# Kernel tuning notes

Hardware: AMD Instinct MI355X
Metric: run time of the kernel (lower is better)

Reference implementation:

```python
import jax, jax.numpy as jnp
import numpy as np

S = 4096      # total packed tokens
B = 8         # number of variable-length segments
E = 1152      # embed_dim (SigLIP2 so400m)
H = 16        # num_heads
D = E // H    # head_dim = 72


def setup_inputs() -> dict:
    key = jax.random.key(0)
    ks = jax.random.split(key, 8)
    w_std = 0.02
    theta = jax.random.uniform(ks[1], (S, D), jnp.float32, 0.0, 2.0 * np.pi)
    return {
        "hidden_states": jax.random.normal(ks[0], (S, E), jnp.float32),
        "cu_seqlens": jnp.arange(B + 1, dtype=jnp.int32) * (S // B),
        "cos": jnp.cos(theta),
        "sin": jnp.sin(theta),
        "Wq": jax.random.normal(ks[2], (E, E), jnp.float32) * w_std,
        "bq": jnp.zeros((E,), jnp.float32),
        "Wk": jax.random.normal(ks[3], (E, E), jnp.float32) * w_std,
        "bk": jnp.zeros((E,), jnp.float32),
        "Wv": jax.random.normal(ks[4], (E, E), jnp.float32) * w_std,
        "bv": jnp.zeros((E,), jnp.float32),
        "Wo": jax.random.normal(ks[5], (E, E), jnp.float32) * w_std,
        "bo": jnp.zeros((E,), jnp.float32),
    }


def _rotate_half(x):
    x1, x2 = jnp.split(x, 2, axis=-1)
    return jnp.concatenate((-x2, x1), axis=-1)


def reference(hidden_states, cu_seqlens, cos, sin, Wq, bq, Wk, bk, Wv, bv, Wo, bo):
    seq_len = hidden_states.shape[0]
    scale = np.float32(D) ** -0.5
    # projections -> [S, H, D]
    q = (hidden_states @ Wq.T + bq).reshape(seq_len, H, D)
    k = (hidden_states @ Wk.T + bk).reshape(seq_len, H, D)
    v = (hidden_states @ Wv.T + bv).reshape(seq_len, H, D)
    # inline RoPE (apply_rotary_pos_emb_vision): cos/sin broadcast over heads
    c = cos[:, None, :]
    s = sin[:, None, :]
    q = q * c + _rotate_half(q) * s
    k = k * c + _rotate_half(k) * s
    # segment id per token from cu_seqlens; block-diagonal attention mask
    seg = jnp.searchsorted(cu_seqlens[1:], jnp.arange(seq_len, dtype=cu_seqlens.dtype), side="right")
    mask = seg[:, None] == seg[None, :]                     # [S, S]
    scores = jnp.einsum("shd,thd->hst", q, k) * scale       # [H, S, S]
    neg = jnp.finfo(scores.dtype).min
    scores = jnp.where(mask[None, :, :], scores, neg)
    probs = jax.nn.softmax(scores, axis=-1)
    attn = jnp.einsum("hst,thd->shd", probs, v).reshape(seq_len, E)
    return attn @ Wo.T + bo
```

## Files before the change

kernel.cpp:

```cpp
#include <hip/hip_runtime.h>
#include <float.h>

#define S_LEN 4096
#define E_DIM 1152
#define NH    16
#define HD    72
#define HD2   36
#define NQKV  3456

typedef __attribute__((ext_vector_type(4))) float f32x4;
typedef __attribute__((ext_vector_type(8))) _Float16 f16x8;

__device__ __forceinline__ unsigned short f2h(float f) {
    union { _Float16 h; unsigned short u; } c;
    c.h = (_Float16)f;
    return c.u;
}

__device__ __forceinline__ void gload_lds16(const unsigned short* g, unsigned short* l) {
    __builtin_amdgcn_global_load_lds(
        (const __attribute__((address_space(1))) unsigned int*)g,
        (__attribute__((address_space(3))) unsigned int*)l, 16, 0, 0);
}

__global__ __launch_bounds__(256)
void pack_f16(const float* __restrict__ hs, const float* __restrict__ wq,
              const float* __restrict__ wk, const float* __restrict__ wv,
              const float* __restrict__ wo,
              unsigned short* __restrict__ hs_h, unsigned short* __restrict__ wqkv_h,
              unsigned short* __restrict__ wo_h)
{
    const float* src; unsigned short* dst; int n4;
    const int WSZ = E_DIM * E_DIM;
    switch (blockIdx.z) {
        case 0: src = hs; dst = hs_h;             n4 = S_LEN * E_DIM / 4; break;
        case 1: src = wq; dst = wqkv_h;           n4 = WSZ / 4; break;
        case 2: src = wk; dst = wqkv_h + WSZ;     n4 = WSZ / 4; break;
        case 3: src = wv; dst = wqkv_h + 2 * WSZ; n4 = WSZ / 4; break;
        default: src = wo; dst = wo_h;            n4 = WSZ / 4; break;
    }
    for (int i = blockIdx.x * 256 + threadIdx.x; i < n4; i += gridDim.x * 256) {
        f32x4 x = ((const f32x4*)src)[i];
        ushort4 hv;
        hv.x = f2h(x[0]); hv.y = f2h(x[1]); hv.z = f2h(x[2]); hv.w = f2h(x[3]);
        ((ushort4*)dst)[i] = hv;
    }
}

__global__ __launch_bounds__(256, 4)
void gemm_qkv_f16(const unsigned short* __restrict__ Ah, const unsigned short* __restrict__ Wh,
                  const float* __restrict__ bq, const float* __restrict__ bk,
                  const float* __restrict__ bv,
                  float* __restrict__ oq, float* __restrict__ ok,
                  unsigned short* __restrict__ vt)
{
    __shared__ unsigned short sA[128 * 64];
    __shared__ unsigned short sB[128 * 64];
    const int tid  = threadIdx.x;
    const int w    = tid >> 6, lane = tid & 63;
    const int quad = lane >> 4, m = lane & 15;
    const int wr   = w & 1,  wc = w >> 1;

    const int bid = blockIdx.x;
    const int lin = (bid & 7) * 108 + (bid >> 3);
    const int n_t = lin >> 5;
    const int m_t = lin & 31;
    const int m0  = m_t * 128;
    const int n0  = n_t * 128;

    const int srow = lane >> 3;
    const int skc  = (lane & 7) ^ srow;

    f32x4 acc[4][4];
    #pragma unroll
    for (int i = 0; i < 4; ++i)
        #pragma unroll
        for (int j = 0; j < 4; ++j) acc[i][j] = (f32x4){0.f, 0.f, 0.f, 0.f};

    const int rm7 = m & 7;

    for (int k0 = 0; k0 < E_DIM; k0 += 64) {
        #pragma unroll
        for (int c = 0; c < 4; ++c) {
            int r = 32 * w + 8 * c + srow;
            gload_lds16(Ah + (size_t)(m0 + r) * E_DIM + k0 + skc * 8, &sA[(32 * w + 8 * c) * 64]);
            gload_lds16(Wh + (size_t)(n0 + r) * E_DIM + k0 + skc * 8, &sB[(32 * w + 8 * c) * 64]);
        }
        __syncthreads();

        #pragma unroll
        for (int k3 = 0; k3 < 2; ++k3) {
            f16x8 ah[4], bh[4];
            #pragma unroll
            for (int t = 0; t < 4; ++t) {
                int pc = ((k3 << 2) + quad) ^ rm7;
                ah[t] = *(const f16x8*)&sA[(64 * wr + 16 * t + m) * 64 + pc * 8];
                bh[t] = *(const f16x8*)&sB[(64 * wc + 16 * t + m) * 64 + pc * 8];
            }
            #pragma unroll
            for (int rt = 0; rt < 4; ++rt)
                #pragma unroll
                for (int ct = 0; ct < 4; ++ct)
                    acc[rt][ct] = __builtin_amdgcn_mfma_f32_16x16x32_f16(ah[rt], bh[ct], acc[rt][ct], 0, 0, 0);
        }
        __syncthreads();
    }

    const int which = n0 / E_DIM;
    const int n0l = n0 - which * E_DIM;
    if (which < 2) {
        const float* bp = (which == 0) ? bq : bk;
        float* Cp       = (which == 0) ? oq : ok;
        #pragma unroll
        for (int ct = 0; ct < 4; ++ct) {
            int col = n0l + 64 * wc + 16 * ct + m;
            float bias = bp[col];
            #pragma unroll
            for (int rt = 0; rt < 4; ++rt)
                #pragma unroll
                for (int reg = 0; reg < 4; ++reg) {
                    int row = m0 + 64 * wr + 16 * rt + 4 * quad + reg;
                    Cp[(size_t)row * E_DIM + col] = acc[rt][ct][reg] + bias;
                }
        }
    } else {
        #pragma unroll
        for (int ct = 0; ct < 4; ++ct) {
            int vcol = n0l + 64 * wc + 16 * ct + m;
            int hh = vcol / HD, dd = vcol - hh * HD;
            float bias = bv[vcol];
            unsigned short* vrow = vt + ((size_t)hh * HD + dd) * S_LEN;
            #pragma unroll
            for (int rt = 0; rt < 4; ++rt) {
                int s0r = m0 + 64 * wr + 16 * rt + 4 * quad;
                ushort4 o;
                o.x = f2h(acc[rt][ct][0] + bias);
                o.y = f2h(acc[rt][ct][1] + bias);
                o.z = f2h(acc[rt][ct][2] + bias);
                o.w = f2h(acc[rt][ct][3] + bias);
                *(ushort4*)&vrow[s0r] = o;
            }
        }
    }
}

__global__ __launch_bounds__(256, 4)
void gemm_out_f16(const unsigned short* __restrict__ Ah, const unsigned short* __restrict__ Wh,
                  const float* __restrict__ bo, float* __restrict__ Cp)
{
    __shared__ unsigned short sA[64 * 64];
    __shared__ unsigned short sB[128 * 64];
    const int tid  = threadIdx.x;
    const int w    = tid >> 6, lane = tid & 63;
    const int quad = lane >> 4, m = lane & 15;
    const int m0   = blockIdx.y * 64;
    const int n0   = blockIdx.x * 128;

    const int srow = lane >> 3;
    const int skc  = (lane & 7) ^ srow;

    f32x4 acc[4][2];
    #pragma unroll
    for (int i = 0; i < 4; ++i)
        #pragma unroll
        for (int j = 0; j < 2; ++j) acc[i][j] = (f32x4){0.f, 0.f, 0.f, 0.f};

    const int rm7 = m & 7;

    for (int k0 = 0; k0 < E_DIM; k0 += 64) {
        #pragma unroll
        for (int c = 0; c < 2; ++c) {
            int r = 16 * w + 8 * c + srow;
            gload_lds16(Ah + (size_t)(m0 + r) * E_DIM + k0 + skc * 8, &sA[(16 * w + 8 * c) * 64]);
        }
        #pragma unroll
        for (int c = 0; c < 4; ++c) {
            int r = 32 * w + 8 * c + srow;
            gload_lds16(Wh + (size_t)(n0 + r) * E_DIM + k0 + skc * 8, &sB[(32 * w + 8 * c) * 64]);
        }
        __syncthreads();
        #pragma unroll
        for (int k3 = 0; k3 < 2; ++k3) {
            f16x8 ah[4], bh[2];
            int pc = ((k3 << 2) + quad) ^ rm7;
            #pragma unroll
            for (int t = 0; t < 4; ++t)
                ah[t] = *(const f16x8*)&sA[(16 * t + m) * 64 + pc * 8];
            #pragma unroll
            for (int ct = 0; ct < 2; ++ct)
                bh[ct] = *(const f16x8*)&sB[(32 * w + 16 * ct + m) * 64 + pc * 8];
            #pragma unroll
            for (int rt = 0; rt < 4; ++rt)
                #pragma unroll
                for (int ct = 0; ct < 2; ++ct)
                    acc[rt][ct] = __builtin_amdgcn_mfma_f32_16x16x32_f16(ah[rt], bh[ct], acc[rt][ct], 0, 0, 0);
        }
        __syncthreads();
    }

    #pragma unroll
    for (int ct = 0; ct < 2; ++ct) {
        int col = n0 + 32 * w + 16 * ct + m;
        float bias = bo[col];
        #pragma unroll
        for (int rt = 0; rt < 4; ++rt)
            #pragma unroll
            for (int reg = 0; reg < 4; ++reg) {
                int row = m0 + 16 * rt + 4 * quad + reg;
                Cp[(size_t)row * E_DIM + col] = acc[rt][ct][reg] + bias;
            }
    }
}

__global__ __launch_bounds__(256)
void prep_k(const float* __restrict__ kf, const float* __restrict__ cosb,
            const float* __restrict__ sinb, unsigned short* __restrict__ kh)
{
    const int h  = blockIdx.y;
    const int s0 = blockIdx.x * 64;
    for (int task = threadIdx.x; task < 64 * 9; task += 256) {
        int row = task / 9, d0 = (task % 9) << 2;
        int s = s0 + row;
        const float* xr = kf + (size_t)s * E_DIM + h * HD;
        f32x4 a  = *(const f32x4*)(xr + d0);
        f32x4 b  = *(const f32x4*)(xr + d0 + HD2);
        f32x4 c1 = *(const f32x4*)(cosb + (size_t)s * HD + d0);
        f32x4 s1 = *(const f32x4*)(sinb + (size_t)s * HD + d0);
        f32x4 c2 = *(const f32x4*)(cosb + (size_t)s * HD + d0 + HD2);
        f32x4 s2 = *(const f32x4*)(sinb + (size_t)s * HD + d0 + HD2);
        f32x4 r1 = a * c1 - b * s1;
        f32x4 r2 = b * c2 + a * s2;
        uint2 u1, u2;
        u1.x = (unsigned)f2h(r1[0]) | ((unsigned)f2h(r1[1]) << 16);
        u1.y = (unsigned)f2h(r1[2]) | ((unsigned)f2h(r1[3]) << 16);
        u2.x = (unsigned)f2h(r2[0]) | ((unsigned)f2h(r2[1]) << 16);
        u2.y = (unsigned)f2h(r2[2]) | ((unsigned)f2h(r2[3]) << 16);
        unsigned short* orow = kh + ((size_t)h * S_LEN + s) * HD;
        *(uint2*)&orow[d0]       = u1;
        *(uint2*)&orow[d0 + HD2] = u2;
    }
}

__global__ __launch_bounds__(256, 4)
void attn_f16(const float* __restrict__ qf, const float* __restrict__ cosb,
              const float* __restrict__ sinb, const unsigned short* __restrict__ kh,
              const unsigned short* __restrict__ vt, const int* __restrict__ cu,
              int nseg, unsigned short* __restrict__ out)
{
    __shared__ unsigned short ks_s[64][72];
    __shared__ unsigned short vs_s[80][72];
    __shared__ unsigned short ss_s[64][72];

    const int tid  = threadIdx.x;
    const int w    = tid >> 6;
    const int lane = tid & 63;
    const int quad = lane >> 4;
    const int m    = lane & 15;
    const int h    = blockIdx.y;
    const int qb0  = blockIdx.x * 64;
    const float cexp = 0.17002324f;

    {
        uint4 zz = make_uint4(0u, 0u, 0u, 0u);
        if (tid < 72) {
            int r = 72 + tid / 9, c = tid % 9;
            *(uint4*)&vs_s[r][c << 3] = zz;
        }
    }

    int rs_r[4], re_r[4];
    #pragma unroll
    for (int reg = 0; reg < 4; ++reg) {
        int row = qb0 + 16 * w + 4 * quad + reg;
        int st = 0;
        for (int i = 1; i < nseg; ++i) if (cu[i] <= row) st = i;
        rs_r[reg] = cu[st];
        re_r[reg] = cu[st + 1];
    }
    int st0 = 0, st1 = 0;
    for (int i = 1; i < nseg; ++i) {
        if (cu[i] <= qb0) st0 = i;
        if (cu[i] <= qb0 + 63) st1 = i;
    }
    const int kstart = cu[st0];
    const int kend   = cu[st1 + 1];
    const bool aligned = (st0 == st1);

    const unsigned short* ktbase = kh + (size_t)h * S_LEN * HD;
    const unsigned short* vtbase = vt + (size_t)h * HD * S_LEN;
    unsigned short* ksf = &ks_s[0][0];

    const int sl0 = tid, sl1 = tid + 256;
    const int sl2 = (tid < 64) ? tid + 512 : tid + 256;
    const int vd0 = sl0 >> 3, vc0 = (sl0 & 7) << 3;
    const int vd1 = sl1 >> 3, vc1 = (sl1 & 7) << 3;
    const int vd2 = sl2 >> 3, vc2 = (sl2 & 7) << 3;

    uint4 kp0, kp1, kp2, vp0, vp1, vp2;
    {
        const unsigned short* kt = ktbase + (size_t)kstart * HD;
        kp0 = *(const uint4*)(kt + sl0 * 8);
        kp1 = *(const uint4*)(kt + sl1 * 8);
        kp2 = *(const uint4*)(kt + sl2 * 8);
        vp0 = *(const uint4*)(vtbase + (size_t)vd0 * S_LEN + kstart + vc0);
        vp1 = *(const uint4*)(vtbase + (size_t)vd1 * S_LEN + kstart + vc1);
        vp2 = *(const uint4*)(vtbase + (size_t)vd2 * S_LEN + kstart + vc2);
    }

    for (int task = tid; task < 64 * 9; task += 256) {
        int row = task / 9, d0 = (task % 9) << 2;
        int s = qb0 + row;
        const float* xr = qf + (size_t)s * E_DIM + h * HD;
        f32x4 a  = *(const f32x4*)(xr + d0);
        f32x4 b  = *(const f32x4*)(xr + d0 + HD2);
        f32x4 c1 = *(const f32x4*)(cosb + (size_t)s * HD + d0);
        f32x4 s1 = *(const f32x4*)(sinb + (size_t)s * HD + d0);
        f32x4 c2 = *(const f32x4*)(cosb + (size_t)s * HD + d0 + HD2);
        f32x4 s2 = *(const f32x4*)(sinb + (size_t)s * HD + d0 + HD2);
        f32x4 r1 = a * c1 - b * s1;
        f32x4 r2 = b * c2 + a * s2;
        uint2 u1, u2;
        u1.x = (unsigned)f2h(r1[0]) | ((unsigned)f2h(r1[1]) << 16);
        u1.y = (unsigned)f2h(r1[2]) | ((unsigned)f2h(r1[3]) << 16);
        u2.x = (unsigned)f2h(r2[0]) | ((unsigned)f2h(r2[1]) << 16);
        u2.y = (unsigned)f2h(r2[2]) | ((unsigned)f2h(r2[3]) << 16);
        *(uint2*)&ks_s[row][d0]       = u1;
        *(uint2*)&ks_s[row][d0 + HD2] = u2;
    }
    __syncthreads();

    f16x8 qfr[3];
    {
        const unsigned short* qrow = &ks_s[16 * w + m][0];
        #pragma unroll
        for (int k3 = 0; k3 < 3; ++k3) {
            bool pad = (k3 == 2) && (quad != 0);
            int off = pad ? 0 : (k3 * 32 + quad * 8);
            f16x8 val = *(const f16x8*)(qrow + off);
            f16x8 z = {0, 0, 0, 0, 0, 0, 0, 0};
            qfr[k3] = pad ? z : val;
        }
    }

    f32x4 acc_o[5];
    #pragma unroll
    for (int i = 0; i < 5; ++i) acc_o[i] = (f32x4){0.f, 0.f, 0.f, 0.f};
    float l_r[4] = {0.f, 0.f, 0.f, 0.f};

    for (int kb = kstart; kb < kend; kb += 64) {
        __syncthreads();
        *(uint4*)(ksf + sl0 * 8) = kp0;
        *(uint4*)(ksf + sl1 * 8) = kp1;
        if (tid < 64) *(uint4*)(ksf + sl2 * 8) = kp2;
        *(uint4*)&vs_s[vd0][vc0] = vp0;
        *(uint4*)&vs_s[vd1][vc1] = vp1;
        if (tid < 64) *(uint4*)&vs_s[vd2][vc2] = vp2;
        __syncthreads();

        int kn = kb + 64;
        if (kn < kend) {
            const unsigned short* kt = ktbase + (size_t)kn * HD;
            kp0 = *(const uint4*)(kt + sl0 * 8);
            kp1 = *(const uint4*)(kt + sl1 * 8);
            kp2 = *(const uint4*)(kt + sl2 * 8);
            vp0 = *(const uint4*)(vtbase + (size_t)vd0 * S_LEN + kn + vc0);
            vp1 = *(const uint4*)(vtbase + (size_t)vd1 * S_LEN + kn + vc1);
            vp2 = *(const uint4*)(vtbase + (size_t)vd2 * S_LEN + kn + vc2);
        }

        f32x4 sacc[4];
        #pragma unroll
        for (int ct = 0; ct < 4; ++ct) sacc[ct] = (f32x4){0.f, 0.f, 0.f, 0.f};
        #pragma unroll
        for (int ct = 0; ct < 4; ++ct) {
            const unsigned short* krow = &ks_s[16 * ct + m][0];
            #pragma unroll
            for (int k3 = 0; k3 < 3; ++k3) {
                bool pad = (k3 == 2) && (quad != 0);
                int off = pad ? 0 : (k3 * 32 + quad * 8);
                f16x8 bfr = *(const f16x8*)(krow + off);
                f16x8 z = {0, 0, 0, 0, 0, 0, 0, 0};
                bfr = pad ? z : bfr;
                sacc[ct] = __builtin_amdgcn_mfma_f32_16x16x32_f16(qfr[k3], bfr, sacc[ct], 0, 0, 0);
            }
        }

        if (aligned) {
            #pragma unroll
            for (int ct = 0; ct < 4; ++ct)
                #pragma unroll
                for (int reg = 0; reg < 4; ++reg) {
                    float p = __builtin_amdgcn_exp2f(sacc[ct][reg] * cexp);
                    l_r[reg] += p;
                    ss_s[16 * w + 4 * quad + reg][16 * ct + m] = f2h(p);
                }
        } else {
            #pragma unroll
            for (int ct = 0; ct < 4; ++ct) {
                int key = kb + 16 * ct + m;
                #pragma unroll
                for (int reg = 0; reg < 4; ++reg) {
                    bool valid = (key >= rs_r[reg]) && (key < re_r[reg]);
                    float p = valid ? __builtin_amdgcn_exp2f(sacc[ct][reg] * cexp) : 0.f;
                    l_r[reg] += p;
                    ss_s[16 * w + 4 * quad + reg][16 * ct + m] = f2h(p);
                }
            }
        }

        {
            const unsigned short* prow = &ss_s[16 * w + m][0];
            f16x8 pf0 = *(const f16x8*)(prow + quad * 8);
            f16x8 pf1 = *(const f16x8*)(prow + 32 + quad * 8);
            #pragma unroll
            for (int ct2 = 0; ct2 < 5; ++ct2) {
                const unsigned short* vrow = &vs_s[16 * ct2 + m][0];
                f16x8 vf0 = *(const f16x8*)(vrow + quad * 8);
                f16x8 vf1 = *(const f16x8*)(vrow + 32 + quad * 8);
                acc_o[ct2] = __builtin_amdgcn_mfma_f32_16x16x32_f16(pf0, vf0, acc_o[ct2], 0, 0, 0);
                acc_o[ct2] = __builtin_amdgcn_mfma_f32_16x16x32_f16(pf1, vf1, acc_o[ct2], 0, 0, 0);
            }
        }
    }

    #pragma unroll
    for (int reg = 0; reg < 4; ++reg) {
        float l = l_r[reg];
        l += __shfl_xor(l, 1);
        l += __shfl_xor(l, 2);
        l += __shfl_xor(l, 4);
        l += __shfl_xor(l, 8);
        l_r[reg] = l;
    }

    #pragma unroll
    for (int reg = 0; reg < 4; ++reg) {
        float linv = (l_r[reg] > 0.f) ? 1.f / l_r[reg] : 0.f;
        int row = qb0 + 16 * w + 4 * quad + reg;
        unsigned short* orow = out + (size_t)row * E_DIM + h * HD;
        #pragma unroll
        for (int ct2 = 0; ct2 < 5; ++ct2) {
            int col = 16 * ct2 + m;
            if (col < HD) orow[col] = f2h(acc_o[ct2][reg] * linv);
        }
    }
}

extern "C" void kernel_launch(void* const* d_in, const int* in_sizes, int n_in,
                              void* d_out, int out_size, void* d_ws, size_t ws_size,
                              hipStream_t stream)
{
    const float* hs   = (const float*)d_in[0];
    const int*   cu   = (const int*)d_in[1];
    const float* cosb = (const float*)d_in[2];
    const float* sinb = (const float*)d_in[3];
    const float* Wq   = (const float*)d_in[4];
    const float* bq   = (const float*)d_in[5];
    const float* Wk   = (const float*)d_in[6];
    const float* bk   = (const float*)d_in[7];
    const float* Wv   = (const float*)d_in[8];
    const float* bv   = (const float*)d_in[9];
    const float* Wo   = (const float*)d_in[10];
    const float* bo   = (const float*)d_in[11];
    float* outp = (float*)d_out;

    const size_t mat = (size_t)S_LEN * E_DIM;
    float* qf = (float*)d_ws;
    float* kf = qf + mat;
    unsigned short* hs_h   = (unsigned short*)(kf + mat);
    unsigned short* wqkv_h = hs_h + mat;
    unsigned short* wo_h   = wqkv_h + (size_t)NQKV * E_DIM;
    unsigned short* vtb    = wo_h + (size_t)E_DIM * E_DIM;
    unsigned short* kh     = hs_h;
    unsigned short* attn_h = (unsigned short*)kf;

    const int nseg = in_sizes[1] - 1;

    dim3 gpack(512, 1, 5);
    pack_f16<<<gpack, 256, 0, stream>>>(hs, Wq, Wk, Wv, Wo, hs_h, wqkv_h, wo_h);

    gemm_qkv_f16<<<dim3(864), 256, 0, stream>>>(hs_h, wqkv_h, bq, bk, bv, qf, kf, vtb);

    dim3 gprep(S_LEN / 64, NH, 1);
    prep_k<<<gprep, 256, 0, stream>>>(kf, cosb, sinb, kh);

    dim3 gattn(S_LEN / 64, NH, 1);
    attn_f16<<<gattn, 256, 0, stream>>>(qf, cosb, sinb, kh, vtb, cu, nseg, attn_h);

    dim3 gout(E_DIM / 128, S_LEN / 64, 1);
    gemm_out_f16<<<gout, 256, 0, stream>>>(attn_h, wo_h, bo, outp);
}
```

Measured before the change: 207.3 us.

## Fuse RoPE and f16 conversion of Q/K into QKV GEMM epilogue

Permutes the Wq/Wk rows during packing so each rotate-half pair lands in adjacent output columns. The QKV GEMM epilogue can then apply RoPE with a lane shuffle and write head-major f16 Q and K directly. This removes the fp32 Q/K round trip, the separate prep_k kernel and the in-attention Q RoPE pass. The cost is scattered 2-byte stores, per-element cos/sin loads in the epilogue, and index arithmetic in the packing loop.

```diff
diff --git a/kernel.cpp b/kernel.cpp
--- a/kernel.cpp
+++ b/kernel.cpp
@@ -32,18 +32,27 @@
 {
     const float* src; unsigned short* dst; int n4;
     const int WSZ = E_DIM * E_DIM;
-    switch (blockIdx.z) {
+    const int z = blockIdx.z;
+    switch (z) {
         case 0: src = hs; dst = hs_h;             n4 = S_LEN * E_DIM / 4; break;
         case 1: src = wq; dst = wqkv_h;           n4 = WSZ / 4; break;
         case 2: src = wk; dst = wqkv_h + WSZ;     n4 = WSZ / 4; break;
         case 3: src = wv; dst = wqkv_h + 2 * WSZ; n4 = WSZ / 4; break;
         default: src = wo; dst = wo_h;            n4 = WSZ / 4; break;
     }
+    const bool perm = (z == 1) || (z == 2);
     for (int i = blockIdx.x * 256 + threadIdx.x; i < n4; i += gridDim.x * 256) {
         f32x4 x = ((const f32x4*)src)[i];
         ushort4 hv;
         hv.x = f2h(x[0]); hv.y = f2h(x[1]); hv.z = f2h(x[2]); hv.w = f2h(x[3]);
-        ((ushort4*)dst)[i] = hv;
+        int o = i;
+        if (perm) {
+            int r = i / 288, cc = i - r * 288;
+            int hh = r / HD, p0 = r - hh * HD;
+            int pr = hh * HD + ((p0 < HD2) ? (p0 << 1) : (((p0 - HD2) << 1) | 1));
+            o = pr * 288 + cc;
+        }
+        ((ushort4*)dst)[o] = hv;
     }
 }
 
@@ -51,7 +60,8 @@
 void gemm_qkv_f16(const unsigned short* __restrict__ Ah, const unsigned short* __restrict__ Wh,
                   const float* __restrict__ bq, const float* __restrict__ bk,
                   const float* __restrict__ bv,
-                  float* __restrict__ oq, float* __restrict__ ok,
+                  const float* __restrict__ cosb, const float* __restrict__ sinb,
+                  unsigned short* __restrict__ qh, unsigned short* __restrict__ khp,
                   unsigned short* __restrict__ vt)
 {
     __shared__ unsigned short sA[128 * 64];
@@ -109,18 +119,26 @@
     const int which = n0 / E_DIM;
     const int n0l = n0 - which * E_DIM;
     if (which < 2) {
-        const float* bp = (which == 0) ? bq : bk;
-        float* Cp       = (which == 0) ? oq : ok;
+        unsigned short* dst = (which == 0) ? qh : khp;
+        const float* bp     = (which == 0) ? bq : bk;
         #pragma unroll
         for (int ct = 0; ct < 4; ++ct) {
-            int col = n0l + 64 * wc + 16 * ct + m;
-            float bias = bp[col];
+            int c = n0l + 64 * wc + 16 * ct + m;
+            int hh = c / HD, p = c - hh * HD;
+            int cidx = (p >> 1) + ((p & 1) ? HD2 : 0);
+            float bias = bp[hh * HD + cidx];
+            float sgn  = (p & 1) ? 1.f : -1.f;
+            unsigned short* hcol = dst + (size_t)hh * S_LEN * HD + p;
             #pragma unroll
             for (int rt = 0; rt < 4; ++rt)
                 #pragma unroll
                 for (int reg = 0; reg < 4; ++reg) {
-                    int row = m0 + 64 * wr + 16 * rt + 4 * quad + reg;
-                    Cp[(size_t)row * E_DIM + col] = acc[rt][ct][reg] + bias;
+                    int s = m0 + 64 * wr + 16 * rt + 4 * quad + reg;
+                    float v  = acc[rt][ct][reg] + bias;
+                    float pv = __shfl_xor(v, 1);
+                    float cs = cosb[(size_t)s * HD + cidx];
+                    float sn = sinb[(size_t)s * HD + cidx];
+                    hcol[(size_t)s * HD] = f2h(v * cs + sgn * pv * sn);
                 }
         }
     } else {
@@ -212,38 +230,8 @@
     }
 }
 
-__global__ __launch_bounds__(256)
-void prep_k(const float* __restrict__ kf, const float* __restrict__ cosb,
-            const float* __restrict__ sinb, unsigned short* __restrict__ kh)
-{
-    const int h  = blockIdx.y;
-    const int s0 = blockIdx.x * 64;
-    for (int task = threadIdx.x; task < 64 * 9; task += 256) {
-        int row = task / 9, d0 = (task % 9) << 2;
-        int s = s0 + row;
-        const float* xr = kf + (size_t)s * E_DIM + h * HD;
-        f32x4 a  = *(const f32x4*)(xr + d0);
-        f32x4 b  = *(const f32x4*)(xr + d0 + HD2);
-        f32x4 c1 = *(const f32x4*)(cosb + (size_t)s * HD + d0);
-        f32x4 s1 = *(const f32x4*)(sinb + (size_t)s * HD + d0);
-        f32x4 c2 = *(const f32x4*)(cosb + (size_t)s * HD + d0 + HD2);
-        f32x4 s2 = *(const f32x4*)(sinb + (size_t)s * HD + d0 + HD2);
-        f32x4 r1 = a * c1 - b * s1;
-        f32x4 r2 = b * c2 + a * s2;
-        uint2 u1, u2;
-        u1.x = (unsigned)f2h(r1[0]) | ((unsigned)f2h(r1[1]) << 16);
-        u1.y = (unsigned)f2h(r1[2]) | ((unsigned)f2h(r1[3]) << 16);
-        u2.x = (unsigned)f2h(r2[0]) | ((unsigned)f2h(r2[1]) << 16);
-        u2.y = (unsigned)f2h(r2[2]) | ((unsigned)f2h(r2[3]) << 16);
-        unsigned short* orow = kh + ((size_t)h * S_LEN + s) * HD;
-        *(uint2*)&orow[d0]       = u1;
-        *(uint2*)&orow[d0 + HD2] = u2;
-    }
-}
-
 __global__ __launch_bounds__(256, 4)
-void attn_f16(const float* __restrict__ qf, const float* __restrict__ cosb,
-              const float* __restrict__ sinb, const unsigned short* __restrict__ kh,
+void attn_f16(const unsigned short* __restrict__ qh, const unsigned short* __restrict__ kh,
               const unsigned short* __restrict__ vt, const int* __restrict__ cu,
               int nseg, unsigned short* __restrict__ out)
 {
@@ -307,31 +295,9 @@
         vp2 = *(const uint4*)(vtbase + (size_t)vd2 * S_LEN + kstart + vc2);
     }
 
-    for (int task = tid; task < 64 * 9; task += 256) {
-        int row = task / 9, d0 = (task % 9) << 2;
-        int s = qb0 + row;
-        const float* xr = qf + (size_t)s * E_DIM + h * HD;
-        f32x4 a  = *(const f32x4*)(xr + d0);
-        f32x4 b  = *(const f32x4*)(xr + d0 + HD2);
-        f32x4 c1 = *(const f32x4*)(cosb + (size_t)s * HD + d0);
-        f32x4 s1 = *(const f32x4*)(sinb + (size_t)s * HD + d0);
-        f32x4 c2 = *(const f32x4*)(cosb + (size_t)s * HD + d0 + HD2);
-        f32x4 s2 = *(const f32x4*)(sinb + (size_t)s * HD + d0 + HD2);
-        f32x4 r1 = a * c1 - b * s1;
-        f32x4 r2 = b * c2 + a * s2;
-        uint2 u1, u2;
-        u1.x = (unsigned)f2h(r1[0]) | ((unsigned)f2h(r1[1]) << 16);
-        u1.y = (unsigned)f2h(r1[2]) | ((unsigned)f2h(r1[3]) << 16);
-        u2.x = (unsigned)f2h(r2[0]) | ((unsigned)f2h(r2[1]) << 16);
-        u2.y = (unsigned)f2h(r2[2]) | ((unsigned)f2h(r2[3]) << 16);
-        *(uint2*)&ks_s[row][d0]       = u1;
-        *(uint2*)&ks_s[row][d0 + HD2] = u2;
-    }
-    __syncthreads();
-
     f16x8 qfr[3];
     {
-        const unsigned short* qrow = &ks_s[16 * w + m][0];
+        const unsigned short* qrow = qh + ((size_t)h * S_LEN + qb0 + 16 * w + m) * HD;
         #pragma unroll
         for (int k3 = 0; k3 < 3; ++k3) {
             bool pad = (k3 == 2) && (quad != 0);
@@ -465,27 +431,24 @@
     float* outp = (float*)d_out;
 
     const size_t mat = (size_t)S_LEN * E_DIM;
-    float* qf = (float*)d_ws;
-    float* kf = qf + mat;
-    unsigned short* hs_h   = (unsigned short*)(kf + mat);
+    unsigned short* hs_h   = (unsigned short*)d_ws;
     unsigned short* wqkv_h = hs_h + mat;
     unsigned short* wo_h   = wqkv_h + (size_t)NQKV * E_DIM;
     unsigned short* vtb    = wo_h + (size_t)E_DIM * E_DIM;
-    unsigned short* kh     = hs_h;
-    unsigned short* attn_h = (unsigned short*)kf;
+    unsigned short* qh     = vtb + mat;
+    unsigned short* kh     = qh + mat;
+    unsigned short* attn_h = kh + mat;
 
     const int nseg = in_sizes[1] - 1;
 
     dim3 gpack(512, 1, 5);
     pack_f16<<<gpack, 256, 0, stream>>>(hs, Wq, Wk, Wv, Wo, hs_h, wqkv_h, wo_h);
 
-    gemm_qkv_f16<<<dim3(864), 256, 0, stream>>>(hs_h, wqkv_h, bq, bk, bv, qf, kf, vtb);
-
-    dim3 gprep(S_LEN / 64, NH, 1);
-    prep_k<<<gprep, 256, 0, stream>>>(kf, cosb, sinb, kh);
+    gemm_qkv_f16<<<dim3(864), 256, 0, stream>>>(hs_h, wqkv_h, bq, bk, bv,
+                                                cosb, sinb, qh, kh, vtb);
 
     dim3 gattn(S_LEN / 64, NH, 1);
-    attn_f16<<<gattn, 256, 0, stream>>>(qf, cosb, sinb, kh, vtb, cu, nseg, attn_h);
+    attn_f16<<<gattn, 256, 0, stream>>>(qh, kh, vtb, cu, nseg, attn_h);
 
     dim3 gout(E_DIM / 128, S_LEN / 64, 1);
     gemm_out_f16<<<gout, 256, 0, stream>>>(attn_h, wo_h, bo, outp);
```

Result: slower. 212.0 us (+2.3%).

## Process two 64-row query tiles per attention block to reuse K/V tiles

Applied to the files above, without the earlier changes.

Each attention workgroup now handles 128 query rows as two 64-row sub-tiles that share every K/V tile staged in LDS. This halves the global-to-LDS K/V traffic and barrier count per query row. In exchange it doubles the accumulator and Q-fragment registers, relaxes the launch bound from 4 to 3 blocks per CU, and halves the grid to 512 blocks, which may lower occupancy and latency hiding.

```diff
diff --git a/kernel.cpp b/kernel.cpp
--- a/kernel.cpp
+++ b/kernel.cpp
@@ -241,7 +241,7 @@
     }
 }
 
-__global__ __launch_bounds__(256, 4)
+__global__ __launch_bounds__(256, 3)
 void attn_f16(const float* __restrict__ qf, const float* __restrict__ cosb,
               const float* __restrict__ sinb, const unsigned short* __restrict__ kh,
               const unsigned short* __restrict__ vt, const int* __restrict__ cu,
@@ -257,7 +257,7 @@
     const int quad = lane >> 4;
     const int m    = lane & 15;
     const int h    = blockIdx.y;
-    const int qb0  = blockIdx.x * 64;
+    const int qb0  = blockIdx.x * 128;
     const float cexp = 0.17002324f;
 
     {
@@ -268,19 +268,21 @@
         }
     }
 
-    int rs_r[4], re_r[4];
-    #pragma unroll
-    for (int reg = 0; reg < 4; ++reg) {
-        int row = qb0 + 16 * w + 4 * quad + reg;
-        int st = 0;
-        for (int i = 1; i < nseg; ++i) if (cu[i] <= row) st = i;
-        rs_r[reg] = cu[st];
-        re_r[reg] = cu[st + 1];
-    }
+    int rs_r[2][4], re_r[2][4];
+    #pragma unroll
+    for (int t = 0; t < 2; ++t)
+        #pragma unroll
+        for (int reg = 0; reg < 4; ++reg) {
+            int row = qb0 + 64 * t + 16 * w + 4 * quad + reg;
+            int st = 0;
+            for (int i = 1; i < nseg; ++i) if (cu[i] <= row) st = i;
+            rs_r[t][reg] = cu[st];
+            re_r[t][reg] = cu[st + 1];
+        }
     int st0 = 0, st1 = 0;
     for (int i = 1; i < nseg; ++i) {
         if (cu[i] <= qb0) st0 = i;
-        if (cu[i] <= qb0 + 63) st1 = i;
+        if (cu[i] <= qb0 + 127) st1 = i;
     }
     const int kstart = cu[st0];
     const int kend   = cu[st1 + 1];
@@ -307,30 +309,31 @@
         vp2 = *(const uint4*)(vtbase + (size_t)vd2 * S_LEN + kstart + vc2);
     }
 
-    for (int task = tid; task < 64 * 9; task += 256) {
-        int row = task / 9, d0 = (task % 9) << 2;
-        int s = qb0 + row;
-        const float* xr = qf + (size_t)s * E_DIM + h * HD;
-        f32x4 a  = *(const f32x4*)(xr + d0);
-        f32x4 b  = *(const f32x4*)(xr + d0 + HD2);
-        f32x4 c1 = *(const f32x4*)(cosb + (size_t)s * HD + d0);
-        f32x4 s1 = *(const f32x4*)(sinb + (size_t)s * HD + d0);
-        f32x4 c2 = *(const f32x4*)(cosb + (size_t)s * HD + d0 + HD2);
-        f32x4 s2 = *(const f32x4*)(sinb + (size_t)s * HD + d0 + HD2);
-        f32x4 r1 = a * c1 - b * s1;
-        f32x4 r2 = b * c2 + a * s2;
-        uint2 u1, u2;
-        u1.x = (unsigned)f2h(r1[0]) | ((unsigned)f2h(r1[1]) << 16);
-        u1.y = (unsigned)f2h(r1[2]) | ((unsigned)f2h(r1[3]) << 16);
-        u2.x = (unsigned)f2h(r2[0]) | ((unsigned)f2h(r2[1]) << 16);
-        u2.y = (unsigned)f2h(r2[2]) | ((unsigned)f2h(r2[3]) << 16);
-        *(uint2*)&ks_s[row][d0]       = u1;
-        *(uint2*)&ks_s[row][d0 + HD2] = u2;
-    }
-    __syncthreads();
-
-    f16x8 qfr[3];
-    {
+    f16x8 qfr[2][3];
+    #pragma unroll
+    for (int t = 0; t < 2; ++t) {
+        if (t) __syncthreads();
+        for (int task = tid; task < 64 * 9; task += 256) {
+            int row = task / 9, d0 = (task % 9) << 2;
+            int s = qb0 + 64 * t + row;
+            const float* xr = qf + (size_t)s * E_DIM + h * HD;
+            f32x4 a  = *(const f32x4*)(xr + d0);
+            f32x4 b  = *(const f32x4*)(xr + d0 + HD2);
+            f32x4 c1 = *(const f32x4*)(cosb + (size_t)s * HD + d0);
+            f32x4 s1 = *(const f32x4*)(sinb + (size_t)s * HD + d0);
+            f32x4 c2 = *(const f32x4*)(cosb + (size_t)s * HD + d0 + HD2);
+            f32x4 s2 = *(const f32x4*)(sinb + (size_t)s * HD + d0 + HD2);
+            f32x4 r1 = a * c1 - b * s1;
+            f32x4 r2 = b * c2 + a * s2;
+            uint2 u1, u2;
+            u1.x = (unsigned)f2h(r1[0]) | ((unsigned)f2h(r1[1]) << 16);
+            u1.y = (unsigned)f2h(r1[2]) | ((unsigned)f2h(r1[3]) << 16);
+            u2.x = (unsigned)f2h(r2[0]) | ((unsigned)f2h(r2[1]) << 16);
+            u2.y = (unsigned)f2h(r2[2]) | ((unsigned)f2h(r2[3]) << 16);
+            *(uint2*)&ks_s[row][d0]       = u1;
+            *(uint2*)&ks_s[row][d0 + HD2] = u2;
+        }
+        __syncthreads();
         const unsigned short* qrow = &ks_s[16 * w + m][0];
         #pragma unroll
         for (int k3 = 0; k3 < 3; ++k3) {
@@ -338,14 +341,16 @@
             int off = pad ? 0 : (k3 * 32 + quad * 8);
             f16x8 val = *(const f16x8*)(qrow + off);
             f16x8 z = {0, 0, 0, 0, 0, 0, 0, 0};
-            qfr[k3] = pad ? z : val;
-        }
-    }
-
-    f32x4 acc_o[5];
-    #pragma unroll
-    for (int i = 0; i < 5; ++i) acc_o[i] = (f32x4){0.f, 0.f, 0.f, 0.f};
-    float l_r[4] = {0.f, 0.f, 0.f, 0.f};
+            qfr[t][k3] = pad ? z : val;
+        }
+    }
+
+    f32x4 acc_o[2][5];
+    #pragma unroll
+    for (int t = 0; t < 2; ++t)
+        #pragma unroll
+        for (int i = 0; i < 5; ++i) acc_o[t][i] = (f32x4){0.f, 0.f, 0.f, 0.f};
+    float l_r[2][4] = {{0.f, 0.f, 0.f, 0.f}, {0.f, 0.f, 0.f, 0.f}};
 
     for (int kb = kstart; kb < kend; kb += 64) {
         __syncthreads();
@@ -368,82 +373,89 @@
             vp2 = *(const uint4*)(vtbase + (size_t)vd2 * S_LEN + kn + vc2);
         }
 
-        f32x4 sacc[4];
-        #pragma unroll
-        for (int ct = 0; ct < 4; ++ct) sacc[ct] = (f32x4){0.f, 0.f, 0.f, 0.f};
-        #pragma unroll
-        for (int ct = 0; ct < 4; ++ct) {
-            const unsigned short* krow = &ks_s[16 * ct + m][0];
-            #pragma unroll
-            for (int k3 = 0; k3 < 3; ++k3) {
-                bool pad = (k3 == 2) && (quad != 0);
-                int off = pad ? 0 : (k3 * 32 + quad * 8);
-                f16x8 bfr = *(const f16x8*)(krow + off);
-                f16x8 z = {0, 0, 0, 0, 0, 0, 0, 0};
-                bfr = pad ? z : bfr;
-                sacc[ct] = __builtin_amdgcn_mfma_f32_16x16x32_f16(qfr[k3], bfr, sacc[ct], 0, 0, 0);
-            }
-        }
-
-        if (aligned) {
-            #pragma unroll
-            for (int ct = 0; ct < 4; ++ct)
-                #pragma unroll
-                for (int reg = 0; reg < 4; ++reg) {
-                    float p = __builtin_amdgcn_exp2f(sacc[ct][reg] * cexp);
-                    l_r[reg] += p;
-                    ss_s[16 * w + 4 * quad + reg][16 * ct + m] = f2h(p);
+        #pragma unroll
+        for (int t = 0; t < 2; ++t) {
+            f32x4 sacc[4];
+            #pragma unroll
+            for (int ct = 0; ct < 4; ++ct) sacc[ct] = (f32x4){0.f, 0.f, 0.f, 0.f};
+            #pragma unroll
+            for (int ct = 0; ct < 4; ++ct) {
+                const unsigned short* krow = &ks_s[16 * ct + m][0];
+                #pragma unroll
+                for (int k3 = 0; k3 < 3; ++k3) {
+                    bool pad = (k3 == 2) && (quad != 0);
+                    int off = pad ? 0 : (k3 * 32 + quad * 8);
+                    f16x8 bfr = *(const f16x8*)(krow + off);
+                    f16x8 z = {0, 0, 0, 0, 0, 0, 0, 0};
+                    bfr = pad ? z : bfr;
+                    sacc[ct] = __builtin_amdgcn_mfma_f32_16x16x32_f16(qfr[t][k3], bfr, sacc[ct], 0, 0, 0);
                 }
-        } else {
-            #pragma unroll
-            for (int ct = 0; ct < 4; ++ct) {
-                int key = kb + 16 * ct + m;
-                #pragma unroll
-                for (int reg = 0; reg < 4; ++reg) {
-                    bool valid = (key >= rs_r[reg]) && (key < re_r[reg]);
-                    float p = valid ? __builtin_amdgcn_exp2f(sacc[ct][reg] * cexp) : 0.f;
-                    l_r[reg] += p;
-                    ss_s[16 * w + 4 * quad + reg][16 * ct + m] = f2h(p);
+            }
+
+            if (aligned) {
+                #pragma unroll
+                for (int ct = 0; ct < 4; ++ct)
+                    #pragma unroll
+                    for (int reg = 0; reg < 4; ++reg) {
+                        float p = __builtin_amdgcn_exp2f(sacc[ct][reg] * cexp);
+                        l_r[t][reg] += p;
+                        ss_s[16 * w + 4 * quad + reg][16 * ct + m] = f2h(p);
+                    }
+            } else {
+                #pragma unroll
+                for (int ct = 0; ct < 4; ++ct) {
+                    int key = kb + 16 * ct + m;
+                    #pragma unroll
+                    for (int reg = 0; reg < 4; ++reg) {
+                        bool valid = (key >= rs_r[t][reg]) && (key < re_r[t][reg]);
+                        float p = valid ? __builtin_amdgcn_exp2f(sacc[ct][reg] * cexp) : 0.f;
+                        l_r[t][reg] += p;
+                        ss_s[16 * w + 4 * quad + reg][16 * ct + m] = f2h(p);
+                    }
                 }
             }
-        }
-
-        {
-            const unsigned short* prow = &ss_s[16 * w + m][0];
-            f16x8 pf0 = *(const f16x8*)(prow + quad * 8);
-            f16x8 pf1 = *(const f16x8*)(prow + 32 + quad * 8);
+
+            {
+                const unsigned short* prow = &ss_s[16 * w + m][0];
+                f16x8 pf0 = *(const f16x8*)(prow + quad * 8);
+                f16x8 pf1 = *(const f16x8*)(prow + 32 + quad * 8);
+                #pragma unroll
+                for (int ct2 = 0; ct2 < 5; ++ct2) {
+                    const unsigned short* vrow = &vs_s[16 * ct2 + m][0];
+                    f16x8 vf0 = *(const f16x8*)(vrow + quad * 8);
+                    f16x8 vf1 = *(const f16x8*)(vrow + 32 + quad * 8);
+                    acc_o[t][ct2] = __builtin_amdgcn_mfma_f32_16x16x32_f16(pf0, vf0, acc_o[t][ct2], 0, 0, 0);
+                    acc_o[t][ct2] = __builtin_amdgcn_mfma_f32_16x16x32_f16(pf1, vf1, acc_o[t][ct2], 0, 0, 0);
+                }
+            }
+        }
+    }
+
+    #pragma unroll
+    for (int t = 0; t < 2; ++t)
+        #pragma unroll
+        for (int reg = 0; reg < 4; ++reg) {
+            float l = l_r[t][reg];
+            l += __shfl_xor(l, 1);
+            l += __shfl_xor(l, 2);
+            l += __shfl_xor(l, 4);
+            l += __shfl_xor(l, 8);
+            l_r[t][reg] = l;
+        }
+
+    #pragma unroll
+    for (int t = 0; t < 2; ++t)
+        #pragma unroll
+        for (int reg = 0; reg < 4; ++reg) {
+            float linv = (l_r[t][reg] > 0.f) ? 1.f / l_r[t][reg] : 0.f;
+            int row = qb0 + 64 * t + 16 * w + 4 * quad + reg;
+            unsigned short* orow = out + (size_t)row * E_DIM + h * HD;
             #pragma unroll
             for (int ct2 = 0; ct2 < 5; ++ct2) {
-                const unsigned short* vrow = &vs_s[16 * ct2 + m][0];
-                f16x8 vf0 = *(const f16x8*)(vrow + quad * 8);
-                f16x8 vf1 = *(const f16x8*)(vrow + 32 + quad * 8);
-                acc_o[ct2] = __builtin_amdgcn_mfma_f32_16x16x32_f16(pf0, vf0, acc_o[ct2], 0, 0, 0);
-                acc_o[ct2] = __builtin_amdgcn_mfma_f32_16x16x32_f16(pf1, vf1, acc_o[ct2], 0, 0, 0);
-            }
-        }
-    }
-
-    #pragma unroll
-    for (int reg = 0; reg < 4; ++reg) {
-        float l = l_r[reg];
-        l += __shfl_xor(l, 1);
-        l += __shfl_xor(l, 2);
-        l += __shfl_xor(l, 4);
-        l += __shfl_xor(l, 8);
-        l_r[reg] = l;
-    }
-
-    #pragma unroll
-    for (int reg = 0; reg < 4; ++reg) {
-        float linv = (l_r[reg] > 0.f) ? 1.f / l_r[reg] : 0.f;
-        int row = qb0 + 16 * w + 4 * quad + reg;
-        unsigned short* orow = out + (size_t)row * E_DIM + h * HD;
-        #pragma unroll
-        for (int ct2 = 0; ct2 < 5; ++ct2) {
-            int col = 16 * ct2 + m;
-            if (col < HD) orow[col] = f2h(acc_o[ct2][reg] * linv);
-        }
-    }
+                int col = 16 * ct2 + m;
+                if (col < HD) orow[col] = f2h(acc_o[t][ct2][reg] * linv);
+            }
+        }
 }
 
 extern "C" void kernel_launch(void* const* d_in, const int* in_sizes, int n_in,
@@ -484,7 +496,7 @@
     dim3 gprep(S_LEN / 64, NH, 1);
     prep_k<<<gprep, 256, 0, stream>>>(kf, cosb, sinb, kh);
 
-    dim3 gattn(S_LEN / 64, NH, 1);
+    dim3 gattn(S_LEN / 128, NH, 1);
     attn_f16<<<gattn, 256, 0, stream>>>(qf, cosb, sinb, kh, vtb, cu, nseg, attn_h);
 
     dim3 gout(E_DIM / 128, S_LEN / 64, 1);
```

Result: slower. 264.5 us (+27.6%).
